# Kernel tuning notes

Measured on AMD Instinct MI355X. Metric: run time of the kernel, lower is better.

Reference implementation:

```python
import jax, jax.numpy as jnp
import numpy as np

B, N, FIN, FOUT = 8, 2048, 128, 128


def setup_inputs() -> dict:
    key = jax.random.key(0)
    k1, k2, k3, k4, k5 = jax.random.split(key, 5)
    x = jax.random.normal(k1, (B, N, FIN), dtype=jnp.float32)
    adj = jax.random.randint(k2, (N, N), 0, 2, dtype=jnp.int32)
    # W stored [in, out] (transpose of torch Linear weight; same math via x @ W)
    W = jax.random.normal(k3, (FIN, FOUT), dtype=jnp.float32) * (1.0 / np.sqrt(FIN))
    # a: Linear(2*out, 1) split into src/dst halves: a([h_i,h_j]) = h_i@a_src + h_j@a_dst
    a_src = jax.random.normal(k4, (FOUT,), dtype=jnp.float32) * 0.1
    a_dst = jax.random.normal(k5, (FOUT,), dtype=jnp.float32) * 0.1
    return {"x": x, "adj": adj, "W": W, "a_src": a_src, "a_dst": a_dst}


def reference(x, adj, W, a_src, a_dst):
    # h: [B, N, FOUT]
    h = jnp.einsum('bnf,fo->bno', x, W)
    # attention logits e_ij = LeakyReLU(a_src.h_i + a_dst.h_j), built by broadcast
    s_i = jnp.einsum('bno,o->bn', h, a_src)  # [B, N]
    s_j = jnp.einsum('bno,o->bn', h, a_dst)  # [B, N]
    e = jax.nn.leaky_relu(s_i[:, :, None] + s_j[:, None, :], negative_slope=0.2)  # [B,N,N]
    scores = jnp.where(adj[None, :, :] == 0, -jnp.inf, e)
    attn = jax.nn.softmax(scores, axis=-1)
    attn = jnp.nan_to_num(attn, nan=0.0)  # rows with no neighbors -> all zeros
    # dropout is identity in eval mode
    out = jnp.einsum('bij,bjo->bio', attn, h)  # [B, N, FOUT]
    return out
```

## Files before the change

kernel.cpp:

```cpp
#include <hip/hip_runtime.h>
#include <math.h>

#define BATCH 8
#define NN 2048
#define FF 128

typedef __attribute__((ext_vector_type(4))) float f32x4;
typedef _Float16 half8 __attribute__((ext_vector_type(8)));

__device__ __forceinline__ unsigned short h2u(_Float16 h) {
    return __builtin_bit_cast(unsigned short, h);
}

__global__ __launch_bounds__(256) void k_h(const float* __restrict__ x,
                                           const int* __restrict__ adj,
                                           const float* __restrict__ W,
                                           const float* __restrict__ a_src,
                                           const float* __restrict__ a_dst,
                                           unsigned short* __restrict__ hF,
                                           float* __restrict__ Eg,  float* __restrict__ E2g,
                                           float* __restrict__ Sg,  float* __restrict__ S2g,
                                           unsigned* __restrict__ amT) {
    __shared__ float sred[4 * 16];
    __shared__ float dred[4 * 16];

    const int t = threadIdx.x;
    const int w = t >> 6, lane = t & 63;
    const int nl = lane & 15, quad = lane >> 4;
    const int row0 = blockIdx.x * 16;
    const int b = row0 >> 11, jloc0 = row0 & 2047;
    const int gr = row0 + nl;
    const int nt0 = w * 2;

    {
        const int prow = blockIdx.x * 2 + (w >> 1);
        const int* __restrict__ ar = adj + (size_t)prow * NN;
        const int s0 = (w & 1) * 16;
        #pragma unroll
        for (int s = 0; s < 16; ++s) {
            const int seg = s0 + s;
            const unsigned long long m = __ballot(ar[seg * 64 + lane] != 0);
            if (lane == 0)  amT[(size_t)(seg * 2) * NN + prow] = (unsigned)m;
            if (lane == 32) amT[(size_t)(seg * 2 + 1) * NN + prow] = (unsigned)(m >> 32);
        }
    }

    f32x4 acc[2] = {{0.f,0.f,0.f,0.f},{0.f,0.f,0.f,0.f}};

    #pragma unroll
    for (int ks = 0; ks < 4; ++ks) {
        const float4 xa = *reinterpret_cast<const float4*>(&x[(size_t)gr * FF + ks * 32 + quad * 8]);
        const float4 xb = *reinterpret_cast<const float4*>(&x[(size_t)gr * FF + ks * 32 + quad * 8 + 4]);
        const float xv[8] = {xa.x, xa.y, xa.z, xa.w, xb.x, xb.y, xb.z, xb.w};
        half8 ah, al;
        #pragma unroll
        for (int i = 0; i < 8; ++i) {
            const _Float16 hh = (_Float16)xv[i];
            ah[i] = hh;
            al[i] = (_Float16)(xv[i] - (float)hh);
        }
        #pragma unroll
        for (int nn = 0; nn < 2; ++nn) {
            const float* __restrict__ wp = W + (size_t)(ks * 32 + quad * 8) * FF + (nt0 + nn) * 16 + nl;
            half8 bh, bl;
            #pragma unroll
            for (int j = 0; j < 8; ++j) {
                const float wv = wp[j * FF];
                const _Float16 hh = (_Float16)wv;
                bh[j] = hh;
                bl[j] = (_Float16)(wv - (float)hh);
            }
            acc[nn] = __builtin_amdgcn_mfma_f32_16x16x32_f16(ah, bh, acc[nn], 0, 0, 0);
            acc[nn] = __builtin_amdgcn_mfma_f32_16x16x32_f16(al, bh, acc[nn], 0, 0, 0);
            acc[nn] = __builtin_amdgcn_mfma_f32_16x16x32_f16(ah, bl, acc[nn], 0, 0, 0);
        }
    }

    const int jloc = jloc0 + quad * 4;
    const int jg = jloc >> 3, u0 = jloc & 7;
    #pragma unroll
    for (int nn = 0; nn < 2; ++nn) {
        ushort4 hv;
        hv.x = h2u((_Float16)acc[nn][0]);
        hv.y = h2u((_Float16)acc[nn][1]);
        hv.z = h2u((_Float16)acc[nn][2]);
        hv.w = h2u((_Float16)acc[nn][3]);
        *reinterpret_cast<ushort4*>(&hF[(size_t)b * 262144 + (nt0 + nn) * 32768 + jg * 128 + nl * 8 + u0]) = hv;
    }

    float as[2], ad[2];
    #pragma unroll
    for (int nn = 0; nn < 2; ++nn) {
        const int col = (nt0 + nn) * 16 + nl;
        as[nn] = a_src[col];
        ad[nn] = a_dst[col];
    }
    #pragma unroll
    for (int r = 0; r < 4; ++r) {
        float sp = acc[0][r] * as[0] + acc[1][r] * as[1];
        float dp = acc[0][r] * ad[0] + acc[1][r] * ad[1];
        #pragma unroll
        for (int off = 8; off >= 1; off >>= 1) {
            sp += __shfl_xor(sp, off, 16);
            dp += __shfl_xor(dp, off, 16);
        }
        if (nl == 0) {
            sred[w * 16 + quad * 4 + r] = sp;
            dred[w * 16 + quad * 4 + r] = dp;
        }
    }
    __syncthreads();
    if (t < 16) {
        const float sp = sred[t] + sred[16 + t] + sred[32 + t] + sred[48 + t];
        const float dp = dred[t] + dred[16 + t] + dred[32 + t] + dred[48 + t];
        const int row = row0 + t;
        Sg[row]  = __expf(sp - 2.f);
        S2g[row] = __expf(0.2f * sp - 2.f);
        Eg[row]  = __expf(dp - 2.f);
        E2g[row] = __expf(0.2f * dp - 2.f);
    }
}

__global__ __launch_bounds__(512, 4) void k_attn(const unsigned short* __restrict__ hF,
                                                 const unsigned* __restrict__ amT,
                                                 const float* __restrict__ Eg,
                                                 const float* __restrict__ E2g,
                                                 const float* __restrict__ Sg,
                                                 const float* __restrict__ S2g,
                                                 float* __restrict__ out) {
    __shared__ unsigned short pA[2 * 32 * 136];
    __shared__ float lred[32];

    const int t = threadIdx.x;
    const int b = blockIdx.y;
    const int i0 = blockIdx.x * 32;

    const int rp = t >> 4, j8 = t & 15;
    const float Si  = Sg[(size_t)b * NN + i0 + rp];
    const float S2i = S2g[(size_t)b * NN + i0 + rp];
    const int bb = (j8 & 3) * 8;
    const int pwo = rp * 136 + j8 * 8;
    const float* __restrict__ Egb  = Eg  + (size_t)b * NN;
    const float* __restrict__ E2gb = E2g + (size_t)b * NN;
    const unsigned* __restrict__ amb = amT + i0 + rp;

    const int w = t >> 6, lane = t & 63;
    const int nl = lane & 15, quad = lane >> 4;
    const unsigned short* __restrict__ hFb = hF + (size_t)b * 262144;
    const int bofs = w * 32768 + quad * 128 + nl * 8;
    int aofs[2];
    #pragma unroll
    for (int mm = 0; mm < 2; ++mm) aofs[mm] = (mm * 16 + nl) * 136 + quad * 8;

    f32x4 acc[2] = {{0.f,0.f,0.f,0.f},{0.f,0.f,0.f,0.f}};
    float la = 0.f;

    for (int tt = 0; tt < 16; ++tt) {
        const int buf = tt & 1;
        const int jofs = tt * 2048;

        half8 bfr[4];
        #pragma unroll
        for (int kk = 0; kk < 4; ++kk)
            bfr[kk] = *reinterpret_cast<const half8*>(hFb + bofs + jofs + kk * 512);

        {
            const int jb = tt * 128 + j8 * 8;
            const float4 e0 = *reinterpret_cast<const float4*>(&Egb[jb]);
            const float4 e1 = *reinterpret_cast<const float4*>(&Egb[jb + 4]);
            const float4 f0 = *reinterpret_cast<const float4*>(&E2gb[jb]);
            const float4 f1 = *reinterpret_cast<const float4*>(&E2gb[jb + 4]);
            const unsigned mw = amb[(size_t)(tt * 4 + (j8 >> 2)) * NN];
            const float ejA[8]  = {e0.x, e0.y, e0.z, e0.w, e1.x, e1.y, e1.z, e1.w};
            const float e2A[8]  = {f0.x, f0.y, f0.z, f0.w, f1.x, f1.y, f1.z, f1.w};
            unsigned short hv[8];
            #pragma unroll
            for (int u = 0; u < 8; ++u) {
                const float v = fmaxf(Si * ejA[u], S2i * e2A[u]);
                const float p = ((mw >> (bb + u)) & 1u) ? v : 0.f;
                la += p;
                hv[u] = h2u((_Float16)p);
            }
            *reinterpret_cast<ushort4*>(&pA[buf * 4352 + pwo])     = *reinterpret_cast<ushort4*>(&hv[0]);
            *reinterpret_cast<ushort4*>(&pA[buf * 4352 + pwo + 4]) = *reinterpret_cast<ushort4*>(&hv[4]);
        }

        __syncthreads();

        half8 afr[2][4];
        #pragma unroll
        for (int mm = 0; mm < 2; ++mm)
            #pragma unroll
            for (int kk = 0; kk < 4; ++kk)
                afr[mm][kk] = *reinterpret_cast<const half8*>(&pA[buf * 4352 + aofs[mm] + kk * 32]);
        #pragma unroll
        for (int kk = 0; kk < 4; ++kk) {
            acc[0] = __builtin_amdgcn_mfma_f32_16x16x32_f16(afr[0][kk], bfr[kk], acc[0], 0, 0, 0);
            acc[1] = __builtin_amdgcn_mfma_f32_16x16x32_f16(afr[1][kk], bfr[kk], acc[1], 0, 0, 0);
        }
    }

    #pragma unroll
    for (int off = 8; off >= 1; off >>= 1) la += __shfl_xor(la, off, 16);
    if (j8 == 0) lred[rp] = la;
    __syncthreads();

    float* __restrict__ ob = out + ((size_t)b * NN + i0) * FF;
    #pragma unroll
    for (int mm = 0; mm < 2; ++mm) {
        #pragma unroll
        for (int r = 0; r < 4; ++r) {
            const int lr = mm * 16 + quad * 4 + r;
            const float l = lred[lr];
            const float inv = (l > 0.f) ? 1.f / l : 0.f;
            ob[(size_t)lr * FF + w * 16 + nl] = acc[mm][r] * inv;
        }
    }
}

extern "C" void kernel_launch(void* const* d_in, const int* in_sizes, int n_in,
                              void* d_out, int out_size, void* d_ws, size_t ws_size,
                              hipStream_t stream) {
    const float* x     = (const float*)d_in[0];
    const int*   adj   = (const int*)d_in[1];
    const float* W     = (const float*)d_in[2];
    const float* a_src = (const float*)d_in[3];
    const float* a_dst = (const float*)d_in[4];
    float* out = (float*)d_out;

    unsigned short* hF = (unsigned short*)d_ws;
    float* Eg  = (float*)(hF + 2097152);
    float* E2g = Eg + 16384;
    float* Sg  = E2g + 16384;
    float* S2g = Sg + 16384;
    unsigned* amT = (unsigned*)(S2g + 16384);

    k_h<<<1024, 256, 0, stream>>>(x, adj, W, a_src, a_dst, hF, Eg, E2g, Sg, S2g, amT);
    k_attn<<<dim3(64, BATCH), 512, 0, stream>>>(hF, amT, Eg, E2g, Sg, S2g, out);
}
```

Before: 109.3 us.

## Enlarge attention tile to 64 rows with split-K across two warp groups

The attention kernel now processes 64 query rows per block with 1024 threads instead of 32 rows with 512. The 16 waves are split into two K-halves that each cover half of every 128-column j tile, and their partial accumulators are reduced through shared memory before the output is written. Each hF B-fragment load now feeds four row tiles instead of two, so global traffic for h is halved. The cost is fewer blocks (256 total), a larger block with higher register and LDS needs, and an extra shared-memory reduction step at the end.

Measured after the change: 115.9 us. 6.1% more time.

```diff
diff --git a/kernel.cpp b/kernel.cpp
--- a/kernel.cpp
+++ b/kernel.cpp
@@ -121,19 +121,19 @@
     }
 }
 
-__global__ __launch_bounds__(512, 4) void k_attn(const unsigned short* __restrict__ hF,
-                                                 const unsigned* __restrict__ amT,
-                                                 const float* __restrict__ Eg,
-                                                 const float* __restrict__ E2g,
-                                                 const float* __restrict__ Sg,
-                                                 const float* __restrict__ S2g,
-                                                 float* __restrict__ out) {
-    __shared__ unsigned short pA[2 * 32 * 136];
-    __shared__ float lred[32];
+__global__ __launch_bounds__(1024) void k_attn(const unsigned short* __restrict__ hF,
+                                               const unsigned* __restrict__ amT,
+                                               const float* __restrict__ Eg,
+                                               const float* __restrict__ E2g,
+                                               const float* __restrict__ Sg,
+                                               const float* __restrict__ S2g,
+                                               float* __restrict__ out) {
+    __shared__ unsigned short pA[2 * 64 * 136];
+    __shared__ float lred[64];
 
     const int t = threadIdx.x;
     const int b = blockIdx.y;
-    const int i0 = blockIdx.x * 32;
+    const int i0 = blockIdx.x * 64;
 
     const int rp = t >> 4, j8 = t & 15;
     const float Si  = Sg[(size_t)b * NN + i0 + rp];
@@ -146,23 +146,24 @@
 
     const int w = t >> 6, lane = t & 63;
     const int nl = lane & 15, quad = lane >> 4;
+    const int nt = w & 7, kh = w >> 3;
     const unsigned short* __restrict__ hFb = hF + (size_t)b * 262144;
-    const int bofs = w * 32768 + quad * 128 + nl * 8;
-    int aofs[2];
-    #pragma unroll
-    for (int mm = 0; mm < 2; ++mm) aofs[mm] = (mm * 16 + nl) * 136 + quad * 8;
-
-    f32x4 acc[2] = {{0.f,0.f,0.f,0.f},{0.f,0.f,0.f,0.f}};
+    const int bofs = nt * 32768 + quad * 128 + nl * 8 + kh * 1024;
+    int aofs[4];
+    #pragma unroll
+    for (int mm = 0; mm < 4; ++mm) aofs[mm] = (mm * 16 + nl) * 136 + quad * 8 + kh * 64;
+
+    f32x4 acc[4] = {{0.f,0.f,0.f,0.f},{0.f,0.f,0.f,0.f},{0.f,0.f,0.f,0.f},{0.f,0.f,0.f,0.f}};
     float la = 0.f;
 
     for (int tt = 0; tt < 16; ++tt) {
         const int buf = tt & 1;
         const int jofs = tt * 2048;
 
-        half8 bfr[4];
-        #pragma unroll
-        for (int kk = 0; kk < 4; ++kk)
-            bfr[kk] = *reinterpret_cast<const half8*>(hFb + bofs + jofs + kk * 512);
+        half8 bfr[2];
+        #pragma unroll
+        for (int kkk = 0; kkk < 2; ++kkk)
+            bfr[kkk] = *reinterpret_cast<const half8*>(hFb + bofs + jofs + kkk * 512);
 
         {
             const int jb = tt * 128 + j8 * 8;
@@ -181,23 +182,23 @@
                 la += p;
                 hv[u] = h2u((_Float16)p);
             }
-            *reinterpret_cast<ushort4*>(&pA[buf * 4352 + pwo])     = *reinterpret_cast<ushort4*>(&hv[0]);
-            *reinterpret_cast<ushort4*>(&pA[buf * 4352 + pwo + 4]) = *reinterpret_cast<ushort4*>(&hv[4]);
+            *reinterpret_cast<ushort4*>(&pA[buf * 8704 + pwo])     = *reinterpret_cast<ushort4*>(&hv[0]);
+            *reinterpret_cast<ushort4*>(&pA[buf * 8704 + pwo + 4]) = *reinterpret_cast<ushort4*>(&hv[4]);
         }
 
         __syncthreads();
 
-        half8 afr[2][4];
-        #pragma unroll
-        for (int mm = 0; mm < 2; ++mm)
-            #pragma unroll
-            for (int kk = 0; kk < 4; ++kk)
-                afr[mm][kk] = *reinterpret_cast<const half8*>(&pA[buf * 4352 + aofs[mm] + kk * 32]);
-        #pragma unroll
-        for (int kk = 0; kk < 4; ++kk) {
-            acc[0] = __builtin_amdgcn_mfma_f32_16x16x32_f16(afr[0][kk], bfr[kk], acc[0], 0, 0, 0);
-            acc[1] = __builtin_amdgcn_mfma_f32_16x16x32_f16(afr[1][kk], bfr[kk], acc[1], 0, 0, 0);
-        }
+        half8 afr[4][2];
+        #pragma unroll
+        for (int mm = 0; mm < 4; ++mm)
+            #pragma unroll
+            for (int kkk = 0; kkk < 2; ++kkk)
+                afr[mm][kkk] = *reinterpret_cast<const half8*>(&pA[buf * 8704 + aofs[mm] + kkk * 32]);
+        #pragma unroll
+        for (int kkk = 0; kkk < 2; ++kkk)
+            #pragma unroll
+            for (int mm = 0; mm < 4; ++mm)
+                acc[mm] = __builtin_amdgcn_mfma_f32_16x16x32_f16(afr[mm][kkk], bfr[kkk], acc[mm], 0, 0, 0);
     }
 
     #pragma unroll
@@ -205,15 +206,27 @@
     if (j8 == 0) lred[rp] = la;
     __syncthreads();
 
-    float* __restrict__ ob = out + ((size_t)b * NN + i0) * FF;
-    #pragma unroll
-    for (int mm = 0; mm < 2; ++mm) {
-        #pragma unroll
-        for (int r = 0; r < 4; ++r) {
-            const int lr = mm * 16 + quad * 4 + r;
-            const float l = lred[lr];
-            const float inv = (l > 0.f) ? 1.f / l : 0.f;
-            ob[(size_t)lr * FF + w * 16 + nl] = acc[mm][r] * inv;
+    float* const Opart = reinterpret_cast<float*>(pA);
+    if (kh == 0) {
+        #pragma unroll
+        for (int mm = 0; mm < 4; ++mm)
+            #pragma unroll
+            for (int r = 0; r < 4; ++r)
+                Opart[(mm * 16 + quad * 4 + r) * 132 + nt * 16 + nl] = acc[mm][r];
+    }
+    __syncthreads();
+    if (kh == 1) {
+        float* __restrict__ ob = out + ((size_t)b * NN + i0) * FF;
+        #pragma unroll
+        for (int mm = 0; mm < 4; ++mm) {
+            #pragma unroll
+            for (int r = 0; r < 4; ++r) {
+                const int lr = mm * 16 + quad * 4 + r;
+                const float l = lred[lr];
+                const float inv = (l > 0.f) ? 1.f / l : 0.f;
+                ob[(size_t)lr * FF + nt * 16 + nl] =
+                    (acc[mm][r] + Opart[lr * 132 + nt * 16 + nl]) * inv;
+            }
         }
     }
 }
@@ -236,5 +249,5 @@
     unsigned* amT = (unsigned*)(S2g + 16384);
 
     k_h<<<1024, 256, 0, stream>>>(x, adj, W, a_src, a_dst, hF, Eg, E2g, Sg, S2g, amT);
-    k_attn<<<dim3(64, BATCH), 512, 0, stream>>>(hF, amT, Eg, E2g, Sg, S2g, out);
-}
+    k_attn<<<dim3(32, BATCH), 1024, 0, stream>>>(hF, amT, Eg, E2g, Sg, S2g, out);
+}
```
